# Kernel tuning notes

Measured on AMD Instinct MI355X. Metric: run time of the kernel, lower is better.

Reference implementation:

```python
import jax, jax.numpy as jnp
import numpy as np

B, C, W, H = 8, 256, 64, 64


def _conv1x1(x, w, b):
    # 1x1 conv == per-pixel channel GEMM. x: [B,C,W,H], w: [O,C], b: [O]
    return jnp.einsum('oc,bchw->bohw', w, x) + b[None, :, None, None]


def setup_inputs() -> dict:
    key = jax.random.key(0)
    ks = jax.random.split(key, 9)
    s = 1.0 / np.sqrt(C)
    return {
        'queries': jax.random.normal(ks[0], (B, C, W, H), dtype=jnp.float32),
        'keys': jax.random.normal(ks[1], (B, C, W, H), dtype=jnp.float32),
        'mask': jax.random.uniform(ks[2], (B, 1, W, H), dtype=jnp.float32),
        'Wq': jax.random.normal(ks[3], (C, C), dtype=jnp.float32) * s,
        'bq': jax.random.normal(ks[4], (C,), dtype=jnp.float32) * 0.01,
        'Wk': jax.random.normal(ks[5], (C, C), dtype=jnp.float32) * s,
        'bk': jax.random.normal(ks[6], (C,), dtype=jnp.float32) * 0.01,
        'Wv': jax.random.normal(ks[7], (C, C), dtype=jnp.float32) * s,
        'bv': jax.random.normal(ks[8], (C,), dtype=jnp.float32) * 0.01,
    }


def reference(queries, keys, mask, Wq, bq, Wk, bk, Wv, bv):
    b, c, w, h = queries.shape
    n = w * h
    q = _conv1x1(queries, Wq, bq).reshape(b, c, n)   # [B,C,N]
    k = _conv1x1(keys, Wk, bk).reshape(b, c, n)      # [B,C,N]
    v = _conv1x1(keys, Wv, bv).reshape(b, c, n)      # [B,C,N]
    # mask spatial size equals feature size -> interpolate(scale_factor=1) is identity
    m = mask.reshape(b, n)                            # [B,N]
    # scores[b,i,j] = <q_i, k_j>; torch's repeated mask multiplies row i by mask[i]
    scores = jnp.einsum('bcq,bck->bqk', q, k) * m[:, :, None]
    attn_w = jax.nn.softmax(scores, axis=-1)          # softmax over key dim
    attn = jnp.einsum('bqk,bck->bcq', attn_w, v).reshape(b, c, w, h)
    return queries * mask + (1.0 - mask) * attn
```

## Files before the change

kernel.cpp:

```cpp
#include <hip/hip_runtime.h>

typedef __attribute__((ext_vector_type(8))) _Float16 half8;
typedef __attribute__((ext_vector_type(4))) _Float16 half4;
typedef __attribute__((ext_vector_type(4))) float f32x4;

#define CDIM 256
#define NDIM 4096
#define MFMAH(a, b, c) __builtin_amdgcn_mfma_f32_16x16x32_f16((a), (b), (c), 0, 0, 0)

#define GLOAD_LDS16(gp, lp)                                              \
  __builtin_amdgcn_global_load_lds(                                      \
      (const __attribute__((address_space(1))) void*)(gp),               \
      (__attribute__((address_space(3))) void*)(lp), 16, 0, 0)

__global__ void cast_w_kernel(const float* __restrict__ Wq,
                              const float* __restrict__ Wk,
                              const float* __restrict__ Wv,
                              _Float16* __restrict__ Wc) {
  int t = blockIdx.x * 256 + threadIdx.x;
  int mat = t >> 14;
  int idx = (t & 16383) * 4;
  const float* W = (mat == 0) ? Wq : (mat == 1 ? Wk : Wv);
  float4 w = *(const float4*)(W + idx);
  half4 h = {(_Float16)w.x, (_Float16)w.y, (_Float16)w.z, (_Float16)w.w};
  *(half4*)(Wc + mat * 65536 + idx) = h;
}

__global__ __launch_bounds__(256, 2) void proj_kernel(
    const float* __restrict__ queries, const float* __restrict__ keys,
    const _Float16* __restrict__ Wc,
    const float* __restrict__ bq, const float* __restrict__ bk,
    const float* __restrict__ bv,
    _Float16* __restrict__ Qh, _Float16* __restrict__ Kh,
    _Float16* __restrict__ Vh)
{
  const int z = blockIdx.z, p = z >> 3, b = z & 7;
  const float* __restrict__ X = (p == 0) ? queries : keys;
  const _Float16* __restrict__ W = Wc + p * 65536;
  const float* __restrict__ bias = (p == 0) ? bq : (p == 1 ? bk : bv);
  const int n0 = blockIdx.x * 128;

  __shared__ __align__(16) _Float16 Xs[128][264];

  const int tid = threadIdx.x;
  const int wv = tid >> 6, lane = tid & 63, l16 = lane & 15, quad = lane >> 4;

#pragma unroll
  for (int it = 0; it < 8; ++it) {
    int id = tid + it * 256;
    int n4 = id & 31, c0 = (id >> 5) * 4;
    const float* Xp = &X[((size_t)(b * CDIM + c0)) * NDIM + n0 + n4 * 4];
    float4 x0 = *(const float4*)(Xp);
    float4 x1 = *(const float4*)(Xp + NDIM);
    float4 x2 = *(const float4*)(Xp + 2 * NDIM);
    float4 x3 = *(const float4*)(Xp + 3 * NDIM);
    const int cs = c0 ^ ((n4 & 7) << 3);
    half4 h;
    h = (half4){(_Float16)x0.x, (_Float16)x1.x, (_Float16)x2.x, (_Float16)x3.x};
    *(half4*)&Xs[n4 * 4 + 0][cs] = h;
    h = (half4){(_Float16)x0.y, (_Float16)x1.y, (_Float16)x2.y, (_Float16)x3.y};
    *(half4*)&Xs[n4 * 4 + 1][cs] = h;
    h = (half4){(_Float16)x0.z, (_Float16)x1.z, (_Float16)x2.z, (_Float16)x3.z};
    *(half4*)&Xs[n4 * 4 + 2][cs] = h;
    h = (half4){(_Float16)x0.w, (_Float16)x1.w, (_Float16)x2.w, (_Float16)x3.w};
    *(half4*)&Xs[n4 * 4 + 3][cs] = h;
  }
  __syncthreads();

  f32x4 acc[4][8];
#pragma unroll
  for (int og = 0; og < 4; ++og)
#pragma unroll
    for (int ng = 0; ng < 8; ++ng) acc[og][ng] = (f32x4){0.f, 0.f, 0.f, 0.f};

#pragma unroll
  for (int kc = 0; kc < 8; ++kc) {
    half8 wf[4], xf[8];
#pragma unroll
    for (int og = 0; og < 4; ++og)
      wf[og] = *(const half8*)(W + (wv * 64 + og * 16 + l16) * CDIM + kc * 32 + quad * 8);
#pragma unroll
    for (int ng = 0; ng < 8; ++ng) {
      const int row = ng * 16 + l16;
      xf[ng] = *(const half8*)&Xs[row][(kc * 32 + quad * 8) ^ (((row >> 2) & 7) << 3)];
    }
#pragma unroll
    for (int og = 0; og < 4; ++og)
#pragma unroll
      for (int ng = 0; ng < 8; ++ng)
        acc[og][ng] = MFMAH(wf[og], xf[ng], acc[og][ng]);
  }

#pragma unroll
  for (int og = 0; og < 4; ++og) {
    float4 b4 = *(const float4*)&bias[wv * 64 + og * 16 + quad * 4];
#pragma unroll
    for (int ng = 0; ng < 8; ++ng) {
      const int n = n0 + ng * 16 + l16;
      if (p == 2) {
#pragma unroll
        for (int r = 0; r < 4; ++r) {
          int o = wv * 64 + og * 16 + quad * 4 + r;
          float y = acc[og][ng][r] + ((const float*)&b4)[r];
          Vh[((size_t)(b * CDIM + o)) * NDIM + n] = (_Float16)y;
        }
      } else {
        half4 h4;
#pragma unroll
        for (int r = 0; r < 4; ++r)
          h4[r] = (_Float16)(acc[og][ng][r] + ((const float*)&b4)[r]);
        size_t idx = ((size_t)(b * NDIM + n)) * CDIM + wv * 64 + og * 16 + quad * 4;
        if (p == 0) *(half4*)&Qh[idx] = h4;
        else        *(half4*)&Kh[idx] = h4;
      }
    }
  }
}

__global__ __launch_bounds__(256, 2) void attn_kernel(
    const float* __restrict__ queries, const float* __restrict__ mask,
    const _Float16* __restrict__ Qh, const _Float16* __restrict__ Kh,
    const _Float16* __restrict__ Vh, float* __restrict__ out)
{
  const int blk = blockIdx.x, b = blk & 7, it = blk >> 3;
  const int i0 = it * 64;

  __shared__ __align__(16) _Float16 Ks[64 * 256];
  __shared__ __align__(16) _Float16 Ps[2][64][72];
  __shared__ __align__(16) float Al[2][64];
  __shared__ __align__(16) float Li[64];

  const int tid = threadIdx.x;
  const int wv = tid >> 6, lane = tid & 63, l16 = lane & 15, quad = lane >> 4;

  const float LOG2E = 1.44269504088896f;

  half8 qf[8];
  {
    const size_t qrow = ((size_t)(b * NDIM + i0 + wv * 16 + l16)) * CDIM;
#pragma unroll
    for (int kc = 0; kc < 8; ++kc)
      qf[kc] = *(const half8*)(Qh + qrow + kc * 32 + quad * 8);
  }
  const float mvalL = mask[(size_t)b * NDIM + i0 + wv * 16 + l16] * LOG2E;
  float m_run = -1e30f, l_run = 0.f;

  f32x4 O[4][4];
#pragma unroll
  for (int g = 0; g < 4; ++g)
#pragma unroll
    for (int cg = 0; cg < 4; ++cg) O[g][cg] = (f32x4){0.f, 0.f, 0.f, 0.f};

  const _Float16* __restrict__ Kb = Kh + (size_t)b * NDIM * CDIM;
  const _Float16* __restrict__ Vw = Vh + ((size_t)(b * CDIM + wv * 64)) * NDIM;

  const int jrow = tid >> 5;
  const int scol = ((tid & 31) * 8) ^ ((jrow & 7) << 3);
  char* const ldst0 = (char*)Ks + (size_t)tid * 16;
  const int kswz = (l16 & 7) << 3;

#pragma unroll
  for (int st = 0; st < 8; ++st)
    GLOAD_LDS16(Kb + (size_t)(st * 8 + jrow) * CDIM + scol, ldst0 + st * 4096);

  for (int jt = 0; jt < 64; ++jt) {
    const int j0 = jt * 64;
    const int pb = jt & 1;
    half8 vf[2][4];
#pragma unroll
    for (int kk = 0; kk < 2; ++kk)
#pragma unroll
      for (int cg = 0; cg < 4; ++cg)
        vf[kk][cg] = *(const half8*)(Vw + (size_t)(cg * 16 + l16) * NDIM + j0 + kk * 32 + quad * 8);
    __syncthreads();

    f32x4 s[4];
#pragma unroll
    for (int js = 0; js < 4; ++js) s[js] = (f32x4){0.f, 0.f, 0.f, 0.f};
#pragma unroll
    for (int kc = 0; kc < 8; ++kc) {
#pragma unroll
      for (int js = 0; js < 4; ++js) {
        half8 kf = *(const half8*)&Ks[(js * 16 + l16) * 256 + ((kc * 32 + quad * 8) ^ kswz)];
        s[js] = MFMAH(kf, qf[kc], s[js]);
      }
    }

    float a[16];
    float mx = -1e30f;
#pragma unroll
    for (int js = 0; js < 4; ++js)
#pragma unroll
      for (int r = 0; r < 4; ++r) {
        float v = s[js][r] * mvalL;
        a[js * 4 + r] = v;
        mx = fmaxf(mx, v);
      }
    mx = fmaxf(mx, __shfl_xor(mx, 16));
    mx = fmaxf(mx, __shfl_xor(mx, 32));
    const float mnew = fmaxf(m_run, mx);
    const float alpha = exp2f(m_run - mnew);
    m_run = mnew;
    float psum = 0.f;
#pragma unroll
    for (int js = 0; js < 4; ++js) {
      float p0 = exp2f(a[js * 4 + 0] - mnew);
      float p1 = exp2f(a[js * 4 + 1] - mnew);
      float p2 = exp2f(a[js * 4 + 2] - mnew);
      float p3 = exp2f(a[js * 4 + 3] - mnew);
      psum += (p0 + p1) + (p2 + p3);
      half4 hp = {(_Float16)p0, (_Float16)p1, (_Float16)p2, (_Float16)p3};
      *(half4*)&Ps[pb][wv * 16 + l16][js * 16 + quad * 4] = hp;
    }
    psum += __shfl_xor(psum, 16);
    psum += __shfl_xor(psum, 32);
    l_run = l_run * alpha + psum;
    if (quad == 0) Al[pb][wv * 16 + l16] = alpha;
    __syncthreads();

    if (jt < 63) {
      const _Float16* srcn = Kb + (size_t)((jt + 1) * 64 + jrow) * CDIM + scol;
#pragma unroll
      for (int st = 0; st < 8; ++st)
        GLOAD_LDS16(srcn + (size_t)st * 8 * CDIM, ldst0 + st * 4096);
    }

    f32x4 av[4];
#pragma unroll
    for (int g = 0; g < 4; ++g) av[g] = *(const f32x4*)&Al[pb][g * 16 + quad * 4];
#pragma unroll
    for (int g = 0; g < 4; ++g)
#pragma unroll
      for (int cg = 0; cg < 4; ++cg)
#pragma unroll
        for (int r = 0; r < 4; ++r) O[g][cg][r] *= av[g][r];
#pragma unroll
    for (int kk = 0; kk < 2; ++kk) {
      half8 pa[4];
#pragma unroll
      for (int g = 0; g < 4; ++g)
        pa[g] = *(const half8*)&Ps[pb][g * 16 + l16][kk * 32 + quad * 8];
#pragma unroll
      for (int g = 0; g < 4; ++g)
#pragma unroll
        for (int cg = 0; cg < 4; ++cg)
          O[g][cg] = MFMAH(pa[g], vf[kk][cg], O[g][cg]);
    }
  }

  if (quad == 0) Li[wv * 16 + l16] = 1.0f / l_run;
  __syncthreads();
#pragma unroll
  for (int g = 0; g < 4; ++g) {
    f32x4 li4 = *(const f32x4*)&Li[g * 16 + quad * 4];
    const int i = i0 + g * 16 + quad * 4;
    float4 m4 = *(const float4*)&mask[(size_t)b * NDIM + i];
#pragma unroll
    for (int cg = 0; cg < 4; ++cg) {
      const int c = wv * 64 + cg * 16 + l16;
      const size_t base = ((size_t)(b * CDIM + c)) * NDIM + i;
      float4 q4 = *(const float4*)(queries + base);
      float4 o4;
      o4.x = q4.x * m4.x + (1.f - m4.x) * (O[g][cg][0] * li4[0]);
      o4.y = q4.y * m4.y + (1.f - m4.y) * (O[g][cg][1] * li4[1]);
      o4.z = q4.z * m4.z + (1.f - m4.z) * (O[g][cg][2] * li4[2]);
      o4.w = q4.w * m4.w + (1.f - m4.w) * (O[g][cg][3] * li4[3]);
      *(float4*)(out + base) = o4;
    }
  }
}

extern "C" void kernel_launch(void* const* d_in, const int* in_sizes, int n_in,
                              void* d_out, int out_size, void* d_ws, size_t ws_size,
                              hipStream_t stream) {
  const float* queries = (const float*)d_in[0];
  const float* keys    = (const float*)d_in[1];
  const float* mask    = (const float*)d_in[2];
  const float* Wq = (const float*)d_in[3];
  const float* bq = (const float*)d_in[4];
  const float* Wk = (const float*)d_in[5];
  const float* bk = (const float*)d_in[6];
  const float* Wv = (const float*)d_in[7];
  const float* bv = (const float*)d_in[8];
  float* out = (float*)d_out;

  const size_t elems = (size_t)8 * NDIM * CDIM;
  _Float16* Qh = (_Float16*)d_ws;
  _Float16* Kh = Qh + elems;
  _Float16* Vh = Kh + elems;
  _Float16* Wc = Vh + elems;

  cast_w_kernel<<<dim3(192), 256, 0, stream>>>(Wq, Wk, Wv, Wc);
  proj_kernel<<<dim3(32, 1, 24), 256, 0, stream>>>(
      queries, keys, Wc, bq, bk, bv, Qh, Kh, Vh);
  attn_kernel<<<dim3(512), 256, 0, stream>>>(
      queries, mask, Qh, Kh, Vh, out);
}
```

Before: 335.6 us.

## Double query tile per block to 128 rows, halving K/V reloads

Result: slower. 386.7 us (+15.2%).

```diff
diff --git a/kernel.cpp b/kernel.cpp
--- a/kernel.cpp
+++ b/kernel.cpp
@@ -117,37 +117,41 @@
   }
 }
 
-__global__ __launch_bounds__(256, 2) void attn_kernel(
+__global__ __launch_bounds__(256, 1) void attn_kernel(
     const float* __restrict__ queries, const float* __restrict__ mask,
     const _Float16* __restrict__ Qh, const _Float16* __restrict__ Kh,
     const _Float16* __restrict__ Vh, float* __restrict__ out)
 {
   const int blk = blockIdx.x, b = blk & 7, it = blk >> 3;
-  const int i0 = it * 64;
+  const int i0 = it * 128;
 
   __shared__ __align__(16) _Float16 Ks[64 * 256];
-  __shared__ __align__(16) _Float16 Ps[2][64][72];
-  __shared__ __align__(16) float Al[2][64];
-  __shared__ __align__(16) float Li[64];
+  __shared__ __align__(16) _Float16 Ps[128][72];
+  __shared__ __align__(16) float Al[128];
+  __shared__ __align__(16) float Li[128];
 
   const int tid = threadIdx.x;
   const int wv = tid >> 6, lane = tid & 63, l16 = lane & 15, quad = lane >> 4;
 
   const float LOG2E = 1.44269504088896f;
 
-  half8 qf[8];
+  half8 qfA[8], qfB[8];
   {
-    const size_t qrow = ((size_t)(b * NDIM + i0 + wv * 16 + l16)) * CDIM;
-#pragma unroll
-    for (int kc = 0; kc < 8; ++kc)
-      qf[kc] = *(const half8*)(Qh + qrow + kc * 32 + quad * 8);
-  }
-  const float mvalL = mask[(size_t)b * NDIM + i0 + wv * 16 + l16] * LOG2E;
-  float m_run = -1e30f, l_run = 0.f;
-
-  f32x4 O[4][4];
-#pragma unroll
-  for (int g = 0; g < 4; ++g)
+    const size_t qrA = ((size_t)(b * NDIM + i0 + wv * 32 + l16)) * CDIM;
+    const size_t qrB = qrA + (size_t)16 * CDIM;
+#pragma unroll
+    for (int kc = 0; kc < 8; ++kc) {
+      qfA[kc] = *(const half8*)(Qh + qrA + kc * 32 + quad * 8);
+      qfB[kc] = *(const half8*)(Qh + qrB + kc * 32 + quad * 8);
+    }
+  }
+  const float mvalA = mask[(size_t)b * NDIM + i0 + wv * 32 + l16] * LOG2E;
+  const float mvalB = mask[(size_t)b * NDIM + i0 + wv * 32 + 16 + l16] * LOG2E;
+  float mA = -1e30f, lA = 0.f, mB = -1e30f, lB = 0.f;
+
+  f32x4 O[8][4];
+#pragma unroll
+  for (int g = 0; g < 8; ++g)
 #pragma unroll
     for (int cg = 0; cg < 4; ++cg) O[g][cg] = (f32x4){0.f, 0.f, 0.f, 0.f};
 
@@ -165,7 +169,6 @@
 
   for (int jt = 0; jt < 64; ++jt) {
     const int j0 = jt * 64;
-    const int pb = jt & 1;
     half8 vf[2][4];
 #pragma unroll
     for (int kk = 0; kk < 2; ++kk)
@@ -174,48 +177,86 @@
         vf[kk][cg] = *(const half8*)(Vw + (size_t)(cg * 16 + l16) * NDIM + j0 + kk * 32 + quad * 8);
     __syncthreads();
 
-    f32x4 s[4];
-#pragma unroll
-    for (int js = 0; js < 4; ++js) s[js] = (f32x4){0.f, 0.f, 0.f, 0.f};
+    f32x4 sA[4], sB[4];
+#pragma unroll
+    for (int js = 0; js < 4; ++js) {
+      sA[js] = (f32x4){0.f, 0.f, 0.f, 0.f};
+      sB[js] = (f32x4){0.f, 0.f, 0.f, 0.f};
+    }
 #pragma unroll
     for (int kc = 0; kc < 8; ++kc) {
 #pragma unroll
       for (int js = 0; js < 4; ++js) {
         half8 kf = *(const half8*)&Ks[(js * 16 + l16) * 256 + ((kc * 32 + quad * 8) ^ kswz)];
-        s[js] = MFMAH(kf, qf[kc], s[js]);
+        sA[js] = MFMAH(kf, qfA[kc], sA[js]);
+        sB[js] = MFMAH(kf, qfB[kc], sB[js]);
       }
     }
 
-    float a[16];
-    float mx = -1e30f;
-#pragma unroll
-    for (int js = 0; js < 4; ++js)
-#pragma unroll
-      for (int r = 0; r < 4; ++r) {
-        float v = s[js][r] * mvalL;
-        a[js * 4 + r] = v;
-        mx = fmaxf(mx, v);
+    {
+      float a[16];
+      float mx = -1e30f;
+#pragma unroll
+      for (int js = 0; js < 4; ++js)
+#pragma unroll
+        for (int r = 0; r < 4; ++r) {
+          float v = sA[js][r] * mvalA;
+          a[js * 4 + r] = v;
+          mx = fmaxf(mx, v);
+        }
+      mx = fmaxf(mx, __shfl_xor(mx, 16));
+      mx = fmaxf(mx, __shfl_xor(mx, 32));
+      const float mnew = fmaxf(mA, mx);
+      const float alpha = exp2f(mA - mnew);
+      mA = mnew;
+      float psum = 0.f;
+#pragma unroll
+      for (int js = 0; js < 4; ++js) {
+        float p0 = exp2f(a[js * 4 + 0] - mnew);
+        float p1 = exp2f(a[js * 4 + 1] - mnew);
+        float p2 = exp2f(a[js * 4 + 2] - mnew);
+        float p3 = exp2f(a[js * 4 + 3] - mnew);
+        psum += (p0 + p1) + (p2 + p3);
+        half4 hp = {(_Float16)p0, (_Float16)p1, (_Float16)p2, (_Float16)p3};
+        *(half4*)&Ps[wv * 32 + l16][js * 16 + quad * 4] = hp;
       }
-    mx = fmaxf(mx, __shfl_xor(mx, 16));
-    mx = fmaxf(mx, __shfl_xor(mx, 32));
-    const float mnew = fmaxf(m_run, mx);
-    const float alpha = exp2f(m_run - mnew);
-    m_run = mnew;
-    float psum = 0.f;
-#pragma unroll
-    for (int js = 0; js < 4; ++js) {
-      float p0 = exp2f(a[js * 4 + 0] - mnew);
-      float p1 = exp2f(a[js * 4 + 1] - mnew);
-      float p2 = exp2f(a[js * 4 + 2] - mnew);
-      float p3 = exp2f(a[js * 4 + 3] - mnew);
-      psum += (p0 + p1) + (p2 + p3);
-      half4 hp = {(_Float16)p0, (_Float16)p1, (_Float16)p2, (_Float16)p3};
-      *(half4*)&Ps[pb][wv * 16 + l16][js * 16 + quad * 4] = hp;
-    }
-    psum += __shfl_xor(psum, 16);
-    psum += __shfl_xor(psum, 32);
-    l_run = l_run * alpha + psum;
-    if (quad == 0) Al[pb][wv * 16 + l16] = alpha;
+      psum += __shfl_xor(psum, 16);
+      psum += __shfl_xor(psum, 32);
+      lA = lA * alpha + psum;
+      if (quad == 0) Al[wv * 32 + l16] = alpha;
+    }
+    {
+      float a[16];
+      float mx = -1e30f;
+#pragma unroll
+      for (int js = 0; js < 4; ++js)
+#pragma unroll
+        for (int r = 0; r < 4; ++r) {
+          float v = sB[js][r] * mvalB;
+          a[js * 4 + r] = v;
+          mx = fmaxf(mx, v);
+        }
+      mx = fmaxf(mx, __shfl_xor(mx, 16));
+      mx = fmaxf(mx, __shfl_xor(mx, 32));
+      const float mnew = fmaxf(mB, mx);
+      const float alpha = exp2f(mB - mnew);
+      mB = mnew;
+      float psum = 0.f;
+#pragma unroll
+      for (int js = 0; js < 4; ++js) {
+        float p0 = exp2f(a[js * 4 + 0] - mnew);
+        float p1 = exp2f(a[js * 4 + 1] - mnew);
+        float p2 = exp2f(a[js * 4 + 2] - mnew);
+        float p3 = exp2f(a[js * 4 + 3] - mnew);
+        psum += (p0 + p1) + (p2 + p3);
+        half4 hp = {(_Float16)p0, (_Float16)p1, (_Float16)p2, (_Float16)p3};
+        *(half4*)&Ps[wv * 32 + 16 + l16][js * 16 + quad * 4] = hp;
+      }
+      psum += __shfl_xor(psum, 16);
+      psum += __shfl_xor(psum, 32);
+      lB = lB * alpha + psum;
+      if (quad == 0) Al[wv * 32 + 16 + l16] = alpha;
+    }
     __syncthreads();
 
     if (jt < 63) {
@@ -225,33 +266,36 @@
         GLOAD_LDS16(srcn + (size_t)st * 8 * CDIM, ldst0 + st * 4096);
     }
 
-    f32x4 av[4];
-#pragma unroll
-    for (int g = 0; g < 4; ++g) av[g] = *(const f32x4*)&Al[pb][g * 16 + quad * 4];
-#pragma unroll
-    for (int g = 0; g < 4; ++g)
+    f32x4 av[8];
+#pragma unroll
+    for (int g = 0; g < 8; ++g) av[g] = *(const f32x4*)&Al[g * 16 + quad * 4];
+#pragma unroll
+    for (int g = 0; g < 8; ++g)
 #pragma unroll
       for (int cg = 0; cg < 4; ++cg)
 #pragma unroll
         for (int r = 0; r < 4; ++r) O[g][cg][r] *= av[g][r];
 #pragma unroll
     for (int kk = 0; kk < 2; ++kk) {
-      half8 pa[4];
-#pragma unroll
-      for (int g = 0; g < 4; ++g)
-        pa[g] = *(const half8*)&Ps[pb][g * 16 + l16][kk * 32 + quad * 8];
-#pragma unroll
-      for (int g = 0; g < 4; ++g)
+      half8 pa[8];
+#pragma unroll
+      for (int g = 0; g < 8; ++g)
+        pa[g] = *(const half8*)&Ps[g * 16 + l16][kk * 32 + quad * 8];
+#pragma unroll
+      for (int g = 0; g < 8; ++g)
 #pragma unroll
         for (int cg = 0; cg < 4; ++cg)
           O[g][cg] = MFMAH(pa[g], vf[kk][cg], O[g][cg]);
     }
   }
 
-  if (quad == 0) Li[wv * 16 + l16] = 1.0f / l_run;
+  if (quad == 0) {
+    Li[wv * 32 + l16] = 1.0f / lA;
+    Li[wv * 32 + 16 + l16] = 1.0f / lB;
+  }
   __syncthreads();
 #pragma unroll
-  for (int g = 0; g < 4; ++g) {
+  for (int g = 0; g < 8; ++g) {
     f32x4 li4 = *(const f32x4*)&Li[g * 16 + quad * 4];
     const int i = i0 + g * 16 + quad * 4;
     float4 m4 = *(const float4*)&mask[(size_t)b * NDIM + i];
@@ -293,6 +337,6 @@
   cast_w_kernel<<<dim3(192), 256, 0, stream>>>(Wq, Wk, Wv, Wc);
   proj_kernel<<<dim3(32, 1, 24), 256, 0, stream>>>(
       queries, keys, Wc, bq, bk, bv, Qh, Kh, Vh);
-  attn_kernel<<<dim3(512), 256, 0, stream>>>(
+  attn_kernel<<<dim3(256), 256, 0, stream>>>(
       queries, mask, Qh, Kh, Vh, out);
 }
```

## Double-buffer K tiles and make each wave own its query rows in PV

Applied to the files above, without the earlier changes.

Result: slower. 672.9 us (+100.5%).

```diff
diff --git a/kernel.cpp b/kernel.cpp
--- a/kernel.cpp
+++ b/kernel.cpp
@@ -122,13 +122,12 @@
     const _Float16* __restrict__ Qh, const _Float16* __restrict__ Kh,
     const _Float16* __restrict__ Vh, float* __restrict__ out)
 {
+  extern __shared__ __align__(16) char smem[];
+  _Float16* const KsB = (_Float16*)smem;
+  _Float16* const Ps  = (_Float16*)(smem + 65536);
+
   const int blk = blockIdx.x, b = blk & 7, it = blk >> 3;
   const int i0 = it * 64;
-
-  __shared__ __align__(16) _Float16 Ks[64 * 256];
-  __shared__ __align__(16) _Float16 Ps[2][64][72];
-  __shared__ __align__(16) float Al[2][64];
-  __shared__ __align__(16) float Li[64];
 
   const int tid = threadIdx.x;
   const int wv = tid >> 6, lane = tid & 63, l16 = lane & 15, quad = lane >> 4;
@@ -142,38 +141,41 @@
     for (int kc = 0; kc < 8; ++kc)
       qf[kc] = *(const half8*)(Qh + qrow + kc * 32 + quad * 8);
   }
-  const float mvalL = mask[(size_t)b * NDIM + i0 + wv * 16 + l16] * LOG2E;
+  const float mv = mask[(size_t)b * NDIM + i0 + wv * 16 + l16];
+  const float mvalL = mv * LOG2E;
   float m_run = -1e30f, l_run = 0.f;
 
-  f32x4 O[4][4];
-#pragma unroll
-  for (int g = 0; g < 4; ++g)
-#pragma unroll
-    for (int cg = 0; cg < 4; ++cg) O[g][cg] = (f32x4){0.f, 0.f, 0.f, 0.f};
+  f32x4 O[16];
+#pragma unroll
+  for (int cg = 0; cg < 16; ++cg) O[cg] = (f32x4){0.f, 0.f, 0.f, 0.f};
 
   const _Float16* __restrict__ Kb = Kh + (size_t)b * NDIM * CDIM;
-  const _Float16* __restrict__ Vw = Vh + ((size_t)(b * CDIM + wv * 64)) * NDIM;
+  const _Float16* __restrict__ Vb = Vh + (size_t)b * CDIM * NDIM;
 
   const int jrow = tid >> 5;
   const int scol = ((tid & 31) * 8) ^ ((jrow & 7) << 3);
-  char* const ldst0 = (char*)Ks + (size_t)tid * 16;
   const int kswz = (l16 & 7) << 3;
 
 #pragma unroll
   for (int st = 0; st < 8; ++st)
-    GLOAD_LDS16(Kb + (size_t)(st * 8 + jrow) * CDIM + scol, ldst0 + st * 4096);
+    GLOAD_LDS16(Kb + (size_t)(st * 8 + jrow) * CDIM + scol,
+                smem + tid * 16 + st * 4096);
 
   for (int jt = 0; jt < 64; ++jt) {
     const int j0 = jt * 64;
     const int pb = jt & 1;
-    half8 vf[2][4];
-#pragma unroll
-    for (int kk = 0; kk < 2; ++kk)
-#pragma unroll
-      for (int cg = 0; cg < 4; ++cg)
-        vf[kk][cg] = *(const half8*)(Vw + (size_t)(cg * 16 + l16) * NDIM + j0 + kk * 32 + quad * 8);
     __syncthreads();
 
+    if (jt < 63) {
+      const _Float16* srcn = Kb + (size_t)((jt + 1) * 64 + jrow) * CDIM + scol;
+      char* dstn = smem + (pb ^ 1) * 32768 + tid * 16;
+#pragma unroll
+      for (int st = 0; st < 8; ++st)
+        GLOAD_LDS16(srcn + (size_t)st * 8 * CDIM, dstn + st * 4096);
+    }
+
+    const _Float16* KsP = KsB + pb * 16384;
+
     f32x4 s[4];
 #pragma unroll
     for (int js = 0; js < 4; ++js) s[js] = (f32x4){0.f, 0.f, 0.f, 0.f};
@@ -181,7 +183,8 @@
     for (int kc = 0; kc < 8; ++kc) {
 #pragma unroll
       for (int js = 0; js < 4; ++js) {
-        half8 kf = *(const half8*)&Ks[(js * 16 + l16) * 256 + ((kc * 32 + quad * 8) ^ kswz)];
+        half8 kf = *(const half8*)&KsP[(js * 16 + l16) * 256 +
+                                       ((kc * 32 + quad * 8) ^ kswz)];
         s[js] = MFMAH(kf, qf[kc], s[js]);
       }
     }
@@ -210,62 +213,37 @@
       float p3 = exp2f(a[js * 4 + 3] - mnew);
       psum += (p0 + p1) + (p2 + p3);
       half4 hp = {(_Float16)p0, (_Float16)p1, (_Float16)p2, (_Float16)p3};
-      *(half4*)&Ps[pb][wv * 16 + l16][js * 16 + quad * 4] = hp;
+      *(half4*)&Ps[(wv * 16 + l16) * 72 + js * 16 + quad * 4] = hp;
     }
     psum += __shfl_xor(psum, 16);
     psum += __shfl_xor(psum, 32);
     l_run = l_run * alpha + psum;
-    if (quad == 0) Al[pb][wv * 16 + l16] = alpha;
-    __syncthreads();
-
-    if (jt < 63) {
-      const _Float16* srcn = Kb + (size_t)((jt + 1) * 64 + jrow) * CDIM + scol;
-#pragma unroll
-      for (int st = 0; st < 8; ++st)
-        GLOAD_LDS16(srcn + (size_t)st * 8 * CDIM, ldst0 + st * 4096);
-    }
-
-    f32x4 av[4];
-#pragma unroll
-    for (int g = 0; g < 4; ++g) av[g] = *(const f32x4*)&Al[pb][g * 16 + quad * 4];
-#pragma unroll
-    for (int g = 0; g < 4; ++g)
-#pragma unroll
-      for (int cg = 0; cg < 4; ++cg)
-#pragma unroll
-        for (int r = 0; r < 4; ++r) O[g][cg][r] *= av[g][r];
-#pragma unroll
-    for (int kk = 0; kk < 2; ++kk) {
-      half8 pa[4];
-#pragma unroll
-      for (int g = 0; g < 4; ++g)
-        pa[g] = *(const half8*)&Ps[pb][g * 16 + l16][kk * 32 + quad * 8];
-#pragma unroll
-      for (int g = 0; g < 4; ++g)
-#pragma unroll
-        for (int cg = 0; cg < 4; ++cg)
-          O[g][cg] = MFMAH(pa[g], vf[kk][cg], O[g][cg]);
-    }
-  }
-
-  if (quad == 0) Li[wv * 16 + l16] = 1.0f / l_run;
-  __syncthreads();
-#pragma unroll
-  for (int g = 0; g < 4; ++g) {
-    f32x4 li4 = *(const f32x4*)&Li[g * 16 + quad * 4];
-    const int i = i0 + g * 16 + quad * 4;
-    float4 m4 = *(const float4*)&mask[(size_t)b * NDIM + i];
-#pragma unroll
-    for (int cg = 0; cg < 4; ++cg) {
-      const int c = wv * 64 + cg * 16 + l16;
-      const size_t base = ((size_t)(b * CDIM + c)) * NDIM + i;
-      float4 q4 = *(const float4*)(queries + base);
-      float4 o4;
-      o4.x = q4.x * m4.x + (1.f - m4.x) * (O[g][cg][0] * li4[0]);
-      o4.y = q4.y * m4.y + (1.f - m4.y) * (O[g][cg][1] * li4[1]);
-      o4.z = q4.z * m4.z + (1.f - m4.z) * (O[g][cg][2] * li4[2]);
-      o4.w = q4.w * m4.w + (1.f - m4.w) * (O[g][cg][3] * li4[3]);
-      *(float4*)(out + base) = o4;
+
+#pragma unroll
+    for (int cg = 0; cg < 16; ++cg)
+#pragma unroll
+      for (int r = 0; r < 4; ++r) O[cg][r] *= alpha;
+    half8 pf0 = *(const half8*)&Ps[(wv * 16 + l16) * 72 + quad * 8];
+    half8 pf1 = *(const half8*)&Ps[(wv * 16 + l16) * 72 + 32 + quad * 8];
+    const _Float16* vrow = Vb + (size_t)l16 * NDIM + j0 + quad * 8;
+#pragma unroll
+    for (int cg = 0; cg < 16; ++cg) {
+      half8 va0 = *(const half8*)(vrow);
+      half8 va1 = *(const half8*)(vrow + 32);
+      O[cg] = MFMAH(va0, pf0, O[cg]);
+      O[cg] = MFMAH(va1, pf1, O[cg]);
+      vrow += (size_t)16 * NDIM;
+    }
+  }
+
+  const float sc = (1.f - mv) / l_run;
+#pragma unroll
+  for (int cg = 0; cg < 16; ++cg) {
+#pragma unroll
+    for (int r = 0; r < 4; ++r) {
+      const int c = cg * 16 + quad * 4 + r;
+      const size_t base = ((size_t)(b * CDIM + c)) * NDIM + i0 + wv * 16 + l16;
+      out[base] = queries[base] * mv + sc * O[cg][r];
     }
   }
 }
@@ -293,6 +271,6 @@
   cast_w_kernel<<<dim3(192), 256, 0, stream>>>(Wq, Wk, Wv, Wc);
   proj_kernel<<<dim3(32, 1, 24), 256, 0, stream>>>(
       queries, keys, Wc, bq, bk, bv, Qh, Kh, Vh);
-  attn_kernel<<<dim3(512), 256, 0, stream>>>(
+  attn_kernel<<<dim3(512), 256, 74752, stream>>>(
       queries, mask, Qh, Kh, Vh, out);
 }
```
